# Optimization experiments

Hardware: AMD Instinct MI355X
Metric: run time of the kernel (lower is better)

The kernel has to match this reference:

```python
import jax, jax.numpy as jnp
import numpy as np

B, S, T = 2048, 32, 32
D, H = 128, 256       # cle_dim, rnn_dim
VS, VT = 256, 256     # source/target char vocab
BOW = 1               # MorphoDataset.Factor.BOW


def setup_inputs() -> dict:
    key = jax.random.key(0)
    ks = jax.random.split(key, 16)
    n = lambda k, sh: (jax.random.normal(k, sh, jnp.float32) * 0.05)
    inp = {
        "src_emb": n(ks[0], (VS, D)),
        "tgt_emb": n(ks[1], (VT, D)),
        "enc_f_W": n(ks[2], (D, 3 * H)),
        "enc_f_U": n(ks[3], (H, 3 * H)),
        "enc_f_b": jnp.zeros((2, 3 * H), jnp.float32),
        "enc_b_W": n(ks[4], (D, 3 * H)),
        "enc_b_U": n(ks[5], (H, 3 * H)),
        "enc_b_b": jnp.zeros((2, 3 * H), jnp.float32),
        "dec_W": n(ks[6], (D + H, 3 * H)),
        "dec_U": n(ks[7], (H, 3 * H)),
        "dec_b": jnp.zeros((2, 3 * H), jnp.float32),
        "out_W": n(ks[8], (H, VT)),
        "out_b": jnp.zeros((VT,), jnp.float32),
        "att_src_W": n(ks[9], (H, H)),
        "att_src_b": jnp.zeros((H,), jnp.float32),
        "att_st_W": n(ks[10], (H, H)),
        "att_st_b": jnp.zeros((H,), jnp.float32),
        "att_v": n(ks[11], (H, 1)),
        "att_v_b": jnp.zeros((1,), jnp.float32),
        "source_ids": jax.random.randint(ks[12], (B, S), 0, VS, jnp.int32),
        "target_ids": jax.random.randint(ks[13], (B, T), 0, VT, jnp.int32),
    }
    return inp


def _gru_step(h, x, W, U, b):
    # Keras GRU, reset_after=True: separate input/recurrent biases b[0], b[1]
    gx = x @ W + b[0]
    gh = h @ U + b[1]
    xz, xr, xh = jnp.split(gx, 3, axis=-1)
    hz, hr, hh = jnp.split(gh, 3, axis=-1)
    z = jax.nn.sigmoid(xz + hz)
    r = jax.nn.sigmoid(xr + hr)
    c = jnp.tanh(xh + r * hh)
    return z * h + (1.0 - z) * c


def _gru_scan(x_tbd, W, U, b):
    # x_tbd: [S, B, D] -> outputs [S, B, H]
    h0 = jnp.zeros((x_tbd.shape[1], U.shape[0]), x_tbd.dtype)
    def step(h, x):
        h = _gru_step(h, x, W, U, b)
        return h, h
    _, ys = jax.lax.scan(step, h0, x_tbd)
    return ys


def reference(src_emb, tgt_emb, enc_f_W, enc_f_U, enc_f_b, enc_b_W, enc_b_U, enc_b_b,
              dec_W, dec_U, dec_b, out_W, out_b, att_src_W, att_src_b,
              att_st_W, att_st_b, att_v, att_v_b, source_ids, target_ids):
    # ---- Encoder: bidirectional GRU, merge_mode='sum' ----
    x = src_emb[source_ids]                      # [B, S, D]
    x_t = jnp.transpose(x, (1, 0, 2))            # [S, B, D]
    fwd = _gru_scan(x_t, enc_f_W, enc_f_U, enc_f_b)
    bwd = _gru_scan(x_t[::-1], enc_b_W, enc_b_U, enc_b_b)[::-1]
    source_states = jnp.transpose(fwd + bwd, (1, 0, 2))  # [B, S, H]

    # projected source states are constant across decoder steps -> precompute
    proj_src = source_states @ att_src_W + att_src_b     # [B, S, H]

    def attend(inp, h):
        p = h @ att_st_W + att_st_b                      # [B, H]
        e = jnp.tanh(proj_src + p[:, None, :]) @ att_v + att_v_b  # [B, S, 1]
        w = jax.nn.softmax(e, axis=1)                    # softmax over source positions
        ctx = jnp.sum(source_states * w, axis=1)         # [B, H]
        return jnp.concatenate([inp, ctx], axis=1)       # [B, D+H]

    # ---- Decoder (teacher forcing) ----
    h0 = source_states[:, 0]                             # [B, H]
    bow = jnp.broadcast_to(tgt_emb[BOW], (source_ids.shape[0], tgt_emb.shape[1]))
    inp0 = attend(bow, h0)

    def dstep(carry, tgt_t):
        h, inp = carry
        h = _gru_step(h, inp, dec_W, dec_U, dec_b)       # GRUCell step
        logits = h @ out_W + out_b                       # [B, VT]
        nxt = attend(tgt_emb[tgt_t], h)
        return (h, nxt), logits

    _, logits = jax.lax.scan(dstep, (h0, inp0), jnp.transpose(target_ids))
    return jnp.transpose(logits, (1, 0, 2))              # [B, T, VT]
```

## Files before the change

### kernel.cpp

```cpp
#include <hip/hip_runtime.h>
#include <math.h>

#define B_  2048
#define S_  32
#define T_  32
#define D_  128
#define H_  256
#define G3  768
#define VT_ 256
#define BOW_ 1

typedef __attribute__((ext_vector_type(8))) short short8;
typedef __attribute__((ext_vector_type(4))) float f32x4;
typedef __attribute__((ext_vector_type(8))) unsigned short us8;
typedef unsigned short u16;

__device__ inline u16 f2bf(float x) {
  union { float f; unsigned u; } v; v.f = x;
  unsigned r = v.u + 0x7FFFu + ((v.u >> 16) & 1u);
  return (u16)(r >> 16);
}
__device__ inline float bf2f(u16 b) {
  union { unsigned u; float f; } v; v.u = ((unsigned)b) << 16; return v.f;
}
__device__ inline int swz(int r) { return ((r ^ (r >> 3)) & 7) << 3; }
__device__ inline float sigm(float x) { return 1.f / (1.f + expf(-x)); }

struct TMat { const float* src; u16* dhi; u16* dlo; int R; int C; int tile0; };
struct TPack { TMat m[10]; };

__global__ __launch_bounds__(256)
void wsplit_t(TPack P) {
  int bx = blockIdx.x;
  TMat M = P.m[0];
  #pragma unroll
  for (int i = 1; i < 10; i++) if (bx >= P.m[i].tile0) M = P.m[i];
  int ti = bx - M.tile0;
  int tilesR = M.R >> 6;
  int rt = ti % tilesR, ct = ti / tilesR;
  int r0 = rt * 64, c0 = ct * 64;
  __shared__ float ts[64][65];
  int tid = threadIdx.x;
  int cx = tid & 63, ry = tid >> 6;
  #pragma unroll
  for (int i = 0; i < 16; i++) {
    int r = ry * 16 + i;
    ts[r][cx] = M.src[(size_t)(r0 + r) * M.C + c0 + cx];
  }
  __syncthreads();
  int rx = tid & 63, cy = tid >> 6;
  #pragma unroll
  for (int i = 0; i < 16; i++) {
    int cc = cy * 16 + i;
    float v = ts[rx][cc];
    u16 hi = f2bf(v);
    size_t o = (size_t)(c0 + cc) * M.R + r0 + rx;
    M.dhi[o] = hi;
    M.dlo[o] = f2bf(v - bf2f(hi));
  }
}

__global__ __launch_bounds__(256)
void esplit(const float* a, const float* b, u16* ah, u16* al, u16* bh, u16* bl, int n) {
  int i = blockIdx.x * 256 + threadIdx.x;
  if (i >= 2 * n) return;
  const float* s = (i < n) ? a : b;
  u16* dh = (i < n) ? ah : bh;
  u16* dl = (i < n) ? al : bl;
  int j = (i < n) ? i : i - n;
  float v = s[j];
  u16 hi = f2bf(v);
  dh[j] = hi; dl[j] = f2bf(v - bf2f(hi));
}

struct PLeg {
  const u16* Ahi; const u16* Alo; int lda;
  const u16* Bthi; const u16* Btlo; int ldb;
  const float* bias; void* C; int ldc; int cmode;
  int M, N, K;
};

__global__ __launch_bounds__(256)
void gemm_pl(PLeg l0, PLeg l1) {
  PLeg L = blockIdx.z ? l1 : l0;
  int n0 = blockIdx.x * 128; if (n0 >= L.N) return;
  int m0 = blockIdx.y * 128; if (m0 >= L.M) return;
  __shared__ u16 As[128 * 64];
  __shared__ u16 Bs[128 * 64];
  int tid = threadIdx.x;
  int lane = tid & 63, wv = tid >> 6;
  int wr = (wv >> 1) * 64, wc = (wv & 1) * 64;
  int fr = lane & 15, fk = (lane >> 4) * 8;
  f32x4 acc[4][4];
  #pragma unroll
  for (int m = 0; m < 4; m++)
    #pragma unroll
    for (int n = 0; n < 4; n++) acc[m][n] = (f32x4){0.f, 0.f, 0.f, 0.f};

  int s_row = tid >> 1, s_part = tid & 1;

  for (int k0 = 0; k0 < L.K; k0 += 32) {
    if (k0) __syncthreads();
    int swA = swz(s_row);
    {
      const u16* src = (s_part ? L.Alo : L.Ahi) + (size_t)(m0 + s_row) * L.lda + k0;
      #pragma unroll
      for (int q = 0; q < 4; q++)
        *(us8*)&As[(s_row * 64 + s_part * 32 + q * 8) ^ swA] = *(const us8*)(src + q * 8);
    }
    {
      const u16* src = (s_part ? L.Btlo : L.Bthi) + (size_t)(n0 + s_row) * L.ldb + k0;
      #pragma unroll
      for (int q = 0; q < 4; q++)
        *(us8*)&Bs[(s_row * 64 + s_part * 32 + q * 8) ^ swA] = *(const us8*)(src + q * 8);
    }
    __syncthreads();
    short8 bhi[4], blo[4];
    #pragma unroll
    for (int n = 0; n < 4; n++) {
      int c = wc + n * 16 + fr; int sw = swz(c);
      bhi[n] = *(const short8*)&Bs[(c * 64 + fk) ^ sw];
      blo[n] = *(const short8*)&Bs[(c * 64 + 32 + fk) ^ sw];
    }
    #pragma unroll
    for (int m = 0; m < 4; m++) {
      int r = wr + m * 16 + fr; int sw = swz(r);
      short8 ahi = *(const short8*)&As[(r * 64 + fk) ^ sw];
      short8 alo = *(const short8*)&As[(r * 64 + 32 + fk) ^ sw];
      #pragma unroll
      for (int n = 0; n < 4; n++) {
        acc[m][n] = __builtin_amdgcn_mfma_f32_16x16x32_bf16(ahi, bhi[n], acc[m][n], 0, 0, 0);
        acc[m][n] = __builtin_amdgcn_mfma_f32_16x16x32_bf16(ahi, blo[n], acc[m][n], 0, 0, 0);
        acc[m][n] = __builtin_amdgcn_mfma_f32_16x16x32_bf16(alo, bhi[n], acc[m][n], 0, 0, 0);
      }
    }
  }
  int rbase = (lane >> 4) * 4;
  #pragma unroll
  for (int m = 0; m < 4; m++)
    #pragma unroll
    for (int rr = 0; rr < 4; rr++) {
      int row = m0 + wr + m * 16 + rbase + rr;
      #pragma unroll
      for (int n = 0; n < 4; n++) {
        int col = n0 + wc + n * 16 + fr;
        float v = acc[m][n][rr];
        if (L.bias) v += L.bias[col];
        if (L.cmode == 0)      ((float*)L.C)[(size_t)row * L.ldc + col] = v;
        else if (L.cmode == 1) ((u16*)L.C)[(size_t)row * L.ldc + col] = f2bf(v);
        else {
          size_t o = (((size_t)(row & (B_ - 1))) * T_ + (row >> 11)) * VT_ + col;
          ((float*)L.C)[o] = v;
        }
      }
    }
}

struct GruDesc {
  const u16 *a0H, *a0L;
  const u16 *a1H, *a1L;
  const u16 *a2H, *a2L;
  const u16 *b0H, *b0L;
  const u16 *b1H, *b1L;
  const u16 *b2H, *b2L;
  const float *bias0, *bias1;
  const float *hold;
  const u16 *holdH, *holdL;
  float *hnew;
  u16 *hh, *hl;
  u16 *ssH, *ssL;
  const int *ids;
  int ssmode;
  int sidx, rev;
};

template<int MODE>
__global__ __launch_bounds__(256)
void gru_step(GruDesc d0, GruDesc d1) {
  GruDesc D = blockIdx.z ? d1 : d0;
  constexpr int KT  = MODE ? 640 : 384;
  constexpr int KT8 = KT / 8;
  __shared__ u16 As[2 * 32 * KT];

  int j0 = blockIdx.x * 64;
  int m0 = blockIdx.y * 32;
  int tid = threadIdx.x;
  int lane = tid & 63, wv = tid >> 6;
  int fr = lane & 15, kq = lane >> 4;
  int jn = j0 + wv * 16 + fr;

  constexpr int SLOTS = 2 * 32 * KT8;
  constexpr int PER_T = SLOTS / 256;
  #pragma unroll
  for (int i = 0; i < PER_T; i++) {
    int s = tid + i * 256;
    int p = s / (32 * KT8);
    int rem = s - p * (32 * KT8);
    int row = rem / KT8;
    int kb = rem - row * KT8;
    int k = kb * 8;
    const u16* src;
    if (MODE == 0) {
      if (k < 256) src = (p ? D.a0L : D.a0H) + (size_t)(m0 + row) * 256 + k;
      else {
        int ar = D.ids[(m0 + row) * S_ + (D.rev ? (S_ - 1 - D.sidx) : D.sidx)];
        src = (p ? D.a1L : D.a1H) + (size_t)ar * 128 + (k - 256);
      }
    } else {
      if (k < 256)      src = (p ? D.a0L : D.a0H) + (size_t)(m0 + row) * 256 + k;
      else if (k < 512) src = (p ? D.a1L : D.a1H) + (size_t)(m0 + row) * 256 + (k - 256);
      else {
        int ar = (D.sidx == 0) ? BOW_ : D.ids[(m0 + row) * T_ + D.sidx - 1];
        src = (p ? D.a2L : D.a2H) + (size_t)ar * 128 + (k - 512);
      }
    }
    *(us8*)&As[(s ^ (row & 7)) * 8] = *(const us8*)src;
  }
  __syncthreads();

  f32x4 acc[4][2];
  #pragma unroll
  for (int a = 0; a < 4; a++)
    #pragma unroll
    for (int m = 0; m < 2; m++) acc[a][m] = (f32x4){0.f, 0.f, 0.f, 0.f};

  int arow_slot[2];
  #pragma unroll
  for (int m = 0; m < 2; m++) arow_slot[m] = (m * 16 + fr) * KT8 + kq;

  auto kstep = [&](int k0, int bk, const u16* bHp, const u16* bLp, int ldb, int ai2) {
    short8 ah[2], al[2];
    #pragma unroll
    for (int m = 0; m < 2; m++) {
      int sl = (arow_slot[m] + (k0 >> 3)) ^ (fr & 7);
      ah[m] = *(const short8*)&As[sl * 8];
      sl = (arow_slot[m] + 32 * KT8 + (k0 >> 3)) ^ (fr & 7);
      al[m] = *(const short8*)&As[sl * 8];
    }
    #pragma unroll
    for (int st = 0; st < 3; st++) {
      size_t ro = (size_t)(st * 256 + jn) * ldb + bk + kq * 8;
      short8 bh = *(const short8*)(bHp + ro);
      short8 bl = *(const short8*)(bLp + ro);
      int ai = (st < 2) ? st : ai2;
      #pragma unroll
      for (int m = 0; m < 2; m++) {
        acc[ai][m] = __builtin_amdgcn_mfma_f32_16x16x32_bf16(ah[m], bh, acc[ai][m], 0, 0, 0);
        acc[ai][m] = __builtin_amdgcn_mfma_f32_16x16x32_bf16(ah[m], bl, acc[ai][m], 0, 0, 0);
        acc[ai][m] = __builtin_amdgcn_mfma_f32_16x16x32_bf16(al[m], bh, acc[ai][m], 0, 0, 0);
      }
    }
  };

  #pragma unroll
  for (int k0 = 0; k0 < 256; k0 += 32) kstep(k0, k0, D.b0H, D.b0L, 256, 2);
  if (MODE == 0) {
    #pragma unroll
    for (int k0 = 256; k0 < 384; k0 += 32) kstep(k0, k0 - 256, D.b1H, D.b1L, 128, 3);
  } else {
    #pragma unroll
    for (int k0 = 256; k0 < 512; k0 += 32) kstep(k0, k0 - 256, D.b1H, D.b1L, 256, 3);
    #pragma unroll
    for (int k0 = 512; k0 < 640; k0 += 32) kstep(k0, k0 - 512, D.b2H, D.b2L, 128, 3);
  }

  int rbase = kq * 4;
  int j = jn;
  float bz = D.bias0[j] + D.bias1[j];
  float br = D.bias0[H_ + j] + D.bias1[H_ + j];
  float bxc = D.bias0[2 * H_ + j];
  float bhc = D.bias1[2 * H_ + j];
  #pragma unroll
  for (int m = 0; m < 2; m++)
    #pragma unroll
    for (int rr = 0; rr < 4; rr++) {
      int b = m0 + m * 16 + rbase + rr;
      size_t o = (size_t)b * H_ + j;
      float z = sigm(acc[0][m][rr] + bz);
      float r = sigm(acc[1][m][rr] + br);
      float c = tanhf(acc[3][m][rr] + bxc + r * (acc[2][m][rr] + bhc));
      float hprev = D.hold ? D.hold[o] : (bf2f(D.holdH[o]) + bf2f(D.holdL[o]));
      float hn = z * hprev + (1.f - z) * c;
      D.hnew[o] = hn;
      u16 hi = f2bf(hn);
      D.hh[o] = hi; D.hl[o] = f2bf(hn - bf2f(hi));
      if (MODE == 0) {
        if (D.ssmode == 1) {
          u16 vh = f2bf(hn);
          D.ssH[o] = vh; D.ssL[o] = f2bf(hn - bf2f(vh));
        } else if (D.ssmode == 2) {
          float v = bf2f(D.ssH[o]) + bf2f(D.ssL[o]) + hn;
          u16 vh = f2bf(v);
          D.ssH[o] = vh; D.ssL[o] = f2bf(v - bf2f(vh));
        }
      }
    }
}

__global__ __launch_bounds__(256)
void attend_k(const u16* __restrict__ projbf, const u16* __restrict__ ssH,
              const float* __restrict__ p, const float* __restrict__ att_v,
              u16* __restrict__ ctxh, u16* __restrict__ ctxl) {
  int b = blockIdx.x;
  int tid = threadIdx.x;
  int lane = tid & 63;
  int wv = tid >> 6;
  __shared__ float e_s[S_];
  __shared__ float w_s[S_];
  float pq[4], vq[4];
  #pragma unroll
  for (int q = 0; q < 4; q++) {
    pq[q] = p[(size_t)b * H_ + q * 64 + lane];
    vq[q] = att_v[q * 64 + lane];
  }
  #pragma unroll
  for (int i = 0; i < 8; i++) {
    int s = wv * 8 + i;
    const u16* pr = projbf + ((size_t)s * B_ + b) * H_;
    float part = 0.f;
    #pragma unroll
    for (int q = 0; q < 4; q++)
      part += tanhf(bf2f(pr[q * 64 + lane]) + pq[q]) * vq[q];
    #pragma unroll
    for (int off = 32; off; off >>= 1)
      part += __shfl_xor(part, off);
    if (lane == 0) e_s[s] = part;
  }
  __syncthreads();
  float m = -1e30f;
  #pragma unroll
  for (int s = 0; s < S_; s++) m = fmaxf(m, e_s[s]);
  float den = 0.f;
  #pragma unroll
  for (int s = 0; s < S_; s++) den += expf(e_s[s] - m);
  if (tid < S_) w_s[tid] = expf(e_s[tid] - m) / den;
  __syncthreads();
  float acc = 0.f;
  #pragma unroll
  for (int s = 0; s < S_; s++)
    acc = fmaf(w_s[s], bf2f(ssH[((size_t)s * B_ + b) * H_ + tid]), acc);
  u16 hi = f2bf(acc);
  size_t o = (size_t)b * H_ + tid;
  ctxh[o] = hi; ctxl[o] = f2bf(acc - bf2f(hi));
}

extern "C" void kernel_launch(void* const* d_in, const int* in_sizes, int n_in,
                              void* d_out, int out_size, void* d_ws, size_t ws_size,
                              hipStream_t stream) {
  const float* src_emb   = (const float*)d_in[0];
  const float* tgt_emb   = (const float*)d_in[1];
  const float* enc_f_W   = (const float*)d_in[2];
  const float* enc_f_U   = (const float*)d_in[3];
  const float* enc_f_b   = (const float*)d_in[4];
  const float* enc_b_W   = (const float*)d_in[5];
  const float* enc_b_U   = (const float*)d_in[6];
  const float* enc_b_b   = (const float*)d_in[7];
  const float* dec_W     = (const float*)d_in[8];
  const float* dec_U     = (const float*)d_in[9];
  const float* dec_b     = (const float*)d_in[10];
  const float* out_W     = (const float*)d_in[11];
  const float* out_b     = (const float*)d_in[12];
  const float* att_src_W = (const float*)d_in[13];
  const float* att_src_b = (const float*)d_in[14];
  const float* att_st_W  = (const float*)d_in[15];
  const float* att_st_b  = (const float*)d_in[16];
  const float* att_v     = (const float*)d_in[17];
  const int* source_ids  = (const int*)d_in[19];
  const int* target_ids  = (const int*)d_in[20];
  float* out = (float*)d_out;

  char* base = (char*)d_ws;
  size_t off = 0;
  auto allocB = [&](size_t bytes) { void* p = base + off; off = (off + bytes + 255) & ~255UL; return p; };
  const size_t BH = (size_t)B_ * H_;

  u16* ssH    = (u16*)allocB((size_t)S_ * BH * 2);
  u16* ssL    = (u16*)allocB((size_t)S_ * BH * 2);
  u16* projbf = (u16*)allocB((size_t)S_ * BH * 2);
  float* pbuf = (float*)allocB(BH * 4);
  u16* ctxh = (u16*)allocB(BH * 2);
  u16* ctxl = (u16*)allocB(BH * 2);

  float* encF0 = (float*)allocB(2 * BH * 4);
  u16*  encPl0 = (u16*)allocB(4 * BH * 2);
  float* encF1 = (float*)allocB(2 * BH * 4);
  u16*  encPl1 = (u16*)allocB(4 * BH * 2);
  float* encF[2][2]  = { { encF0, encF0 + BH }, { encF1, encF1 + BH } };
  u16*  encH[2][2]   = { { encPl0, encPl0 + 2 * BH }, { encPl1, encPl1 + 2 * BH } };
  u16*  encL[2][2]   = { { encPl0 + BH, encPl0 + 3 * BH }, { encPl1 + BH, encPl1 + 3 * BH } };

  float* hDecF[2] = { (float*)allocB(BH * 4), (float*)allocB(BH * 4) };
  u16* hAllH = (u16*)allocB((size_t)T_ * BH * 2);
  u16* hAllL = (u16*)allocB((size_t)T_ * BH * 2);

  auto planes2 = [&](size_t n, u16*& h, u16*& l) { h = (u16*)allocB(n * 2); l = (u16*)allocB(n * 2); };
  u16 *UtFh,*UtFl,*UtBh,*UtBl,*WtFh,*WtFl,*WtBh,*WtBl;
  u16 *dUth,*dUtl,*dWcth,*dWctl,*dWxth,*dWxtl;
  u16 *oWth,*oWtl,*aStth,*aSttl,*aSrth,*aSrtl;
  u16 *sEh,*sEl,*tEh,*tEl;
  planes2((size_t)G3*H_, UtFh, UtFl);   planes2((size_t)G3*H_, UtBh, UtBl);
  planes2((size_t)G3*D_, WtFh, WtFl);   planes2((size_t)G3*D_, WtBh, WtBl);
  planes2((size_t)G3*H_, dUth, dUtl);   planes2((size_t)G3*H_, dWcth, dWctl);
  planes2((size_t)G3*D_, dWxth, dWxtl);
  planes2((size_t)H_*VT_, oWth, oWtl);
  planes2((size_t)H_*H_, aStth, aSttl); planes2((size_t)H_*H_, aSrth, aSrtl);
  planes2((size_t)VT_*D_, sEh, sEl);    planes2((size_t)VT_*D_, tEh, tEl);

  TPack P;
  P.m[0] = { enc_f_U,          UtFh, UtFl, 256, 768, 0   };
  P.m[1] = { enc_b_U,          UtBh, UtBl, 256, 768, 48  };
  P.m[2] = { dec_U,            dUth, dUtl, 256, 768, 96  };
  P.m[3] = { dec_W + 128 * G3, dWcth, dWctl, 256, 768, 144 };
  P.m[4] = { enc_f_W,          WtFh, WtFl, 128, 768, 192 };
  P.m[5] = { enc_b_W,          WtBh, WtBl, 128, 768, 216 };
  P.m[6] = { dec_W,            dWxth, dWxtl, 128, 768, 240 };
  P.m[7] = { out_W,            oWth, oWtl, 256, 256, 264 };
  P.m[8] = { att_st_W,         aStth, aSttl, 256, 256, 280 };
  P.m[9] = { att_src_W,        aSrth, aSrtl, 256, 256, 296 };
  wsplit_t<<<312, 256, 0, stream>>>(P);
  esplit<<<(2 * VT_ * D_ + 255) / 256, 256, 0, stream>>>(src_emb, tgt_emb, sEh, sEl, tEh, tEl, VT_ * D_);

  hipMemsetAsync(encF0, 0, 2 * BH * 4, stream);
  hipMemsetAsync(encPl0, 0, 4 * BH * 2, stream);

  for (int s = 0; s < S_; s++) {
    int p = s & 1;
    GruDesc dd[2];
    for (int d = 0; d < 2; d++) {
      GruDesc& D = dd[d];
      D.a0H = encH[p][d]; D.a0L = encL[p][d];
      D.a1H = sEh; D.a1L = sEl;
      D.a2H = nullptr; D.a2L = nullptr;
      D.b0H = d ? UtBh : UtFh; D.b0L = d ? UtBl : UtFl;
      D.b1H = d ? WtBh : WtFh; D.b1L = d ? WtBl : WtFl;
      D.b2H = nullptr; D.b2L = nullptr;
      D.bias0 = d ? enc_b_b : enc_f_b;
      D.bias1 = (d ? enc_b_b : enc_f_b) + G3;
      D.hold = encF[p][d]; D.holdH = nullptr; D.holdL = nullptr;
      D.hnew = encF[p ^ 1][d];
      D.hh = encH[p ^ 1][d]; D.hl = encL[p ^ 1][d];
      int pos = d ? (S_ - 1 - s) : s;
      D.ssH = ssH + (size_t)pos * BH; D.ssL = ssL + (size_t)pos * BH;
      D.ids = source_ids;
      D.ssmode = (s < S_ / 2) ? 1 : 2;
      D.sidx = s; D.rev = d;
    }
    gru_step<0><<<dim3(4, 64, 2), 256, 0, stream>>>(dd[0], dd[1]);
  }

  {
    PLeg proj = { ssH, ssL, H_, aSrth, aSrtl, H_, att_src_b, projbf, H_, 1, S_ * B_, H_, H_ };
    PLeg p0   = { ssH, ssL, H_, aStth, aSttl, H_, att_st_b,  pbuf,   H_, 0, B_,      H_, H_ };
    gemm_pl<<<dim3(2, 512, 2), 256, 0, stream>>>(proj, p0);
  }
  attend_k<<<B_, 256, 0, stream>>>(projbf, ssH, pbuf, att_v, ctxh, ctxl);

  for (int t = 0; t < T_; t++) {
    int p = t & 1;
    GruDesc D = {};
    D.a0H = t ? hAllH + (size_t)(t - 1) * BH : ssH;
    D.a0L = t ? hAllL + (size_t)(t - 1) * BH : ssL;
    D.a1H = ctxh; D.a1L = ctxl;
    D.a2H = tEh;  D.a2L = tEl;
    D.b0H = dUth;  D.b0L = dUtl;
    D.b1H = dWcth; D.b1L = dWctl;
    D.b2H = dWxth; D.b2L = dWxtl;
    D.bias0 = dec_b; D.bias1 = dec_b + G3;
    if (t == 0) { D.hold = nullptr; D.holdH = ssH; D.holdL = ssL; }
    else        { D.hold = hDecF[p]; D.holdH = nullptr; D.holdL = nullptr; }
    D.hnew = hDecF[p ^ 1];
    D.hh = hAllH + (size_t)t * BH; D.hl = hAllL + (size_t)t * BH;
    D.ssH = nullptr; D.ssL = nullptr;
    D.ids = target_ids;
    D.ssmode = 0; D.sidx = t; D.rev = 0;
    gru_step<1><<<dim3(4, 64, 1), 256, 0, stream>>>(D, D);

    if (t < T_ - 1) {
      PLeg LP = { hAllH + (size_t)t * BH, hAllL + (size_t)t * BH, H_,
                  aStth, aSttl, H_, att_st_b, pbuf, H_, 0, B_, H_, H_ };
      gemm_pl<<<dim3(2, 16, 1), 256, 0, stream>>>(LP, LP);
      attend_k<<<B_, 256, 0, stream>>>(projbf, ssH, pbuf, att_v, ctxh, ctxl);
    }
  }

  {
    PLeg LO = { hAllH, hAllL, H_, oWth, oWtl, H_, out_b, out, 0, 2, T_ * B_, VT_, H_ };
    gemm_pl<<<dim3(2, 512, 1), 256, 0, stream>>>(LO, LO);
  }
}
```

Baseline: 3.648 ms.

## Prefetch operands in registers across GEMM, GRU step and attention kernels

The tiled GEMM now loads the next K-chunk from global memory into registers while MFMAs run on the current shared-memory tile, at the cost of an extra barrier per chunk. The GRU step kernel drops its shared-memory staging of A and instead reads A and B fragments straight from global memory with a two-deep register double buffer. The decoder GRU launch now uses 16-row tiles, which doubles the grid. The attention kernel issues all projection and source-state loads up front to expose memory-level parallelism, which raises register pressure.

```diff
diff --git a/kernel.cpp b/kernel.cpp
--- a/kernel.cpp
+++ b/kernel.cpp
@@ -98,29 +98,38 @@
     for (int n = 0; n < 4; n++) acc[m][n] = (f32x4){0.f, 0.f, 0.f, 0.f};
 
   int s_row = tid >> 1, s_part = tid & 1;
-
-  for (int k0 = 0; k0 < L.K; k0 += 32) {
-    if (k0) __syncthreads();
-    int swA = swz(s_row);
-    {
-      const u16* src = (s_part ? L.Alo : L.Ahi) + (size_t)(m0 + s_row) * L.lda + k0;
+  const u16* srcA = (s_part ? L.Alo : L.Ahi) + (size_t)(m0 + s_row) * L.lda;
+  const u16* srcB = (s_part ? L.Btlo : L.Bthi) + (size_t)(n0 + s_row) * L.ldb;
+
+  us8 ra[4], rb[4];
+  #pragma unroll
+  for (int q = 0; q < 4; q++) {
+    ra[q] = *(const us8*)(srcA + q * 8);
+    rb[q] = *(const us8*)(srcB + q * 8);
+  }
+
+  int NC = L.K / 32;
+  int swA = swz(s_row);
+  for (int c = 0; c < NC; c++) {
+    #pragma unroll
+    for (int q = 0; q < 4; q++) {
+      *(us8*)&As[(s_row * 64 + s_part * 32 + q * 8) ^ swA] = ra[q];
+      *(us8*)&Bs[(s_row * 64 + s_part * 32 + q * 8) ^ swA] = rb[q];
+    }
+    __syncthreads();
+    if (c + 1 < NC) {
       #pragma unroll
-      for (int q = 0; q < 4; q++)
-        *(us8*)&As[(s_row * 64 + s_part * 32 + q * 8) ^ swA] = *(const us8*)(src + q * 8);
-    }
-    {
-      const u16* src = (s_part ? L.Btlo : L.Bthi) + (size_t)(n0 + s_row) * L.ldb + k0;
-      #pragma unroll
-      for (int q = 0; q < 4; q++)
-        *(us8*)&Bs[(s_row * 64 + s_part * 32 + q * 8) ^ swA] = *(const us8*)(src + q * 8);
-    }
-    __syncthreads();
+      for (int q = 0; q < 4; q++) {
+        ra[q] = *(const us8*)(srcA + (c + 1) * 32 + q * 8);
+        rb[q] = *(const us8*)(srcB + (c + 1) * 32 + q * 8);
+      }
+    }
     short8 bhi[4], blo[4];
     #pragma unroll
     for (int n = 0; n < 4; n++) {
-      int c = wc + n * 16 + fr; int sw = swz(c);
-      bhi[n] = *(const short8*)&Bs[(c * 64 + fk) ^ sw];
-      blo[n] = *(const short8*)&Bs[(c * 64 + 32 + fk) ^ sw];
+      int cc = wc + n * 16 + fr; int sw = swz(cc);
+      bhi[n] = *(const short8*)&Bs[(cc * 64 + fk) ^ sw];
+      blo[n] = *(const short8*)&Bs[(cc * 64 + 32 + fk) ^ sw];
     }
     #pragma unroll
     for (int m = 0; m < 4; m++) {
@@ -134,6 +143,7 @@
         acc[m][n] = __builtin_amdgcn_mfma_f32_16x16x32_bf16(alo, bhi[n], acc[m][n], 0, 0, 0);
       }
     }
+    __syncthreads();
   }
   int rbase = (lane >> 4) * 4;
   #pragma unroll
@@ -178,107 +188,97 @@
 __global__ __launch_bounds__(256)
 void gru_step(GruDesc d0, GruDesc d1) {
   GruDesc D = blockIdx.z ? d1 : d0;
-  constexpr int KT  = MODE ? 640 : 384;
-  constexpr int KT8 = KT / 8;
-  __shared__ u16 As[2 * 32 * KT];
+  constexpr int MF  = MODE ? 1 : 2;
+  constexpr int NST = MODE ? 20 : 12;
 
   int j0 = blockIdx.x * 64;
-  int m0 = blockIdx.y * 32;
+  int m0 = blockIdx.y * (16 * MF);
   int tid = threadIdx.x;
   int lane = tid & 63, wv = tid >> 6;
   int fr = lane & 15, kq = lane >> 4;
   int jn = j0 + wv * 16 + fr;
 
-  constexpr int SLOTS = 2 * 32 * KT8;
-  constexpr int PER_T = SLOTS / 256;
-  #pragma unroll
-  for (int i = 0; i < PER_T; i++) {
-    int s = tid + i * 256;
-    int p = s / (32 * KT8);
-    int rem = s - p * (32 * KT8);
-    int row = rem / KT8;
-    int kb = rem - row * KT8;
-    int k = kb * 8;
-    const u16* src;
+  int hrow[MF], erow[MF];
+  #pragma unroll
+  for (int mf = 0; mf < MF; mf++) {
+    hrow[mf] = m0 + mf * 16 + fr;
+    if (MODE == 0)
+      erow[mf] = D.ids[hrow[mf] * S_ + (D.rev ? (S_ - 1 - D.sidx) : D.sidx)];
+    else
+      erow[mf] = (D.sidx == 0) ? BOW_ : D.ids[hrow[mf] * T_ + D.sidx - 1];
+  }
+
+  f32x4 acc[4][MF];
+  #pragma unroll
+  for (int a = 0; a < 4; a++)
+    #pragma unroll
+    for (int mf = 0; mf < MF; mf++) acc[a][mf] = (f32x4){0.f, 0.f, 0.f, 0.f};
+
+  short8 pah[2][MF], pal[2][MF], pbh[2][3], pbl[2][3];
+
+  auto loadStep = [&](int i, short8* ah, short8* al, short8* bh3, short8* bl3) {
+    const u16 *BH, *BL, *AH, *AL; int ldb, bk, lda; bool gather;
     if (MODE == 0) {
-      if (k < 256) src = (p ? D.a0L : D.a0H) + (size_t)(m0 + row) * 256 + k;
-      else {
-        int ar = D.ids[(m0 + row) * S_ + (D.rev ? (S_ - 1 - D.sidx) : D.sidx)];
-        src = (p ? D.a1L : D.a1H) + (size_t)ar * 128 + (k - 256);
-      }
+      if (i < 8) { BH = D.b0H; BL = D.b0L; ldb = 256; bk = i * 32;
+                   AH = D.a0H; AL = D.a0L; lda = 256; gather = false; }
+      else       { BH = D.b1H; BL = D.b1L; ldb = 128; bk = (i - 8) * 32;
+                   AH = D.a1H; AL = D.a1L; lda = 128; gather = true; }
     } else {
-      if (k < 256)      src = (p ? D.a0L : D.a0H) + (size_t)(m0 + row) * 256 + k;
-      else if (k < 512) src = (p ? D.a1L : D.a1H) + (size_t)(m0 + row) * 256 + (k - 256);
-      else {
-        int ar = (D.sidx == 0) ? BOW_ : D.ids[(m0 + row) * T_ + D.sidx - 1];
-        src = (p ? D.a2L : D.a2H) + (size_t)ar * 128 + (k - 512);
-      }
-    }
-    *(us8*)&As[(s ^ (row & 7)) * 8] = *(const us8*)src;
-  }
-  __syncthreads();
-
-  f32x4 acc[4][2];
-  #pragma unroll
-  for (int a = 0; a < 4; a++)
-    #pragma unroll
-    for (int m = 0; m < 2; m++) acc[a][m] = (f32x4){0.f, 0.f, 0.f, 0.f};
-
-  int arow_slot[2];
-  #pragma unroll
-  for (int m = 0; m < 2; m++) arow_slot[m] = (m * 16 + fr) * KT8 + kq;
-
-  auto kstep = [&](int k0, int bk, const u16* bHp, const u16* bLp, int ldb, int ai2) {
-    short8 ah[2], al[2];
-    #pragma unroll
-    for (int m = 0; m < 2; m++) {
-      int sl = (arow_slot[m] + (k0 >> 3)) ^ (fr & 7);
-      ah[m] = *(const short8*)&As[sl * 8];
-      sl = (arow_slot[m] + 32 * KT8 + (k0 >> 3)) ^ (fr & 7);
-      al[m] = *(const short8*)&As[sl * 8];
+      if (i < 8)       { BH = D.b0H; BL = D.b0L; ldb = 256; bk = i * 32;
+                         AH = D.a0H; AL = D.a0L; lda = 256; gather = false; }
+      else if (i < 16) { BH = D.b1H; BL = D.b1L; ldb = 256; bk = (i - 8) * 32;
+                         AH = D.a1H; AL = D.a1L; lda = 256; gather = false; }
+      else             { BH = D.b2H; BL = D.b2L; ldb = 128; bk = (i - 16) * 32;
+                         AH = D.a2H; AL = D.a2L; lda = 128; gather = true; }
+    }
+    #pragma unroll
+    for (int mf = 0; mf < MF; mf++) {
+      int r = gather ? erow[mf] : hrow[mf];
+      size_t ao = (size_t)r * lda + bk + kq * 8;
+      ah[mf] = *(const short8*)(AH + ao);
+      al[mf] = *(const short8*)(AL + ao);
     }
     #pragma unroll
     for (int st = 0; st < 3; st++) {
       size_t ro = (size_t)(st * 256 + jn) * ldb + bk + kq * 8;
-      short8 bh = *(const short8*)(bHp + ro);
-      short8 bl = *(const short8*)(bLp + ro);
+      bh3[st] = *(const short8*)(BH + ro);
+      bl3[st] = *(const short8*)(BL + ro);
+    }
+  };
+
+  loadStep(0, pah[0], pal[0], pbh[0], pbl[0]);
+  loadStep(1, pah[1], pal[1], pbh[1], pbl[1]);
+  #pragma unroll
+  for (int i = 0; i < NST; i++) {
+    int ai2 = (i < 8) ? 2 : 3;
+    #pragma unroll
+    for (int st = 0; st < 3; st++) {
       int ai = (st < 2) ? st : ai2;
       #pragma unroll
-      for (int m = 0; m < 2; m++) {
-        acc[ai][m] = __builtin_amdgcn_mfma_f32_16x16x32_bf16(ah[m], bh, acc[ai][m], 0, 0, 0);
-        acc[ai][m] = __builtin_amdgcn_mfma_f32_16x16x32_bf16(ah[m], bl, acc[ai][m], 0, 0, 0);
-        acc[ai][m] = __builtin_amdgcn_mfma_f32_16x16x32_bf16(al[m], bh, acc[ai][m], 0, 0, 0);
+      for (int mf = 0; mf < MF; mf++) {
+        acc[ai][mf] = __builtin_amdgcn_mfma_f32_16x16x32_bf16(pah[i & 1][mf], pbh[i & 1][st], acc[ai][mf], 0, 0, 0);
+        acc[ai][mf] = __builtin_amdgcn_mfma_f32_16x16x32_bf16(pah[i & 1][mf], pbl[i & 1][st], acc[ai][mf], 0, 0, 0);
+        acc[ai][mf] = __builtin_amdgcn_mfma_f32_16x16x32_bf16(pal[i & 1][mf], pbh[i & 1][st], acc[ai][mf], 0, 0, 0);
       }
     }
-  };
-
-  #pragma unroll
-  for (int k0 = 0; k0 < 256; k0 += 32) kstep(k0, k0, D.b0H, D.b0L, 256, 2);
-  if (MODE == 0) {
-    #pragma unroll
-    for (int k0 = 256; k0 < 384; k0 += 32) kstep(k0, k0 - 256, D.b1H, D.b1L, 128, 3);
-  } else {
-    #pragma unroll
-    for (int k0 = 256; k0 < 512; k0 += 32) kstep(k0, k0 - 256, D.b1H, D.b1L, 256, 3);
-    #pragma unroll
-    for (int k0 = 512; k0 < 640; k0 += 32) kstep(k0, k0 - 512, D.b2H, D.b2L, 128, 3);
+    if (i + 2 < NST) loadStep(i + 2, pah[i & 1], pal[i & 1], pbh[i & 1], pbl[i & 1]);
   }
 
   int rbase = kq * 4;
   int j = jn;
-  float bz = D.bias0[j] + D.bias1[j];
-  float br = D.bias0[H_ + j] + D.bias1[H_ + j];
+  float bz  = D.bias0[j] + D.bias1[j];
+  float br  = D.bias0[H_ + j] + D.bias1[H_ + j];
   float bxc = D.bias0[2 * H_ + j];
   float bhc = D.bias1[2 * H_ + j];
   #pragma unroll
-  for (int m = 0; m < 2; m++)
+  for (int mf = 0; mf < MF; mf++)
     #pragma unroll
     for (int rr = 0; rr < 4; rr++) {
-      int b = m0 + m * 16 + rbase + rr;
+      int b = m0 + mf * 16 + rbase + rr;
       size_t o = (size_t)b * H_ + j;
-      float z = sigm(acc[0][m][rr] + bz);
-      float r = sigm(acc[1][m][rr] + br);
-      float c = tanhf(acc[3][m][rr] + bxc + r * (acc[2][m][rr] + bhc));
+      float z = sigm(acc[0][mf][rr] + bz);
+      float r = sigm(acc[1][mf][rr] + br);
+      float c = tanhf(acc[3][mf][rr] + bxc + r * (acc[2][mf][rr] + bhc));
       float hprev = D.hold ? D.hold[o] : (bf2f(D.holdH[o]) + bf2f(D.holdL[o]));
       float hn = z * hprev + (1.f - z) * c;
       D.hnew[o] = hn;
@@ -313,18 +313,27 @@
     pq[q] = p[(size_t)b * H_ + q * 64 + lane];
     vq[q] = att_v[q * 64 + lane];
   }
+  float pv[8][4];
   #pragma unroll
   for (int i = 0; i < 8; i++) {
-    int s = wv * 8 + i;
-    const u16* pr = projbf + ((size_t)s * B_ + b) * H_;
+    const u16* pr = projbf + ((size_t)(wv * 8 + i) * B_ + b) * H_;
+    #pragma unroll
+    for (int q = 0; q < 4; q++) pv[i][q] = bf2f(pr[q * 64 + lane]);
+  }
+  u16 sv[S_];
+  #pragma unroll
+  for (int s = 0; s < S_; s++) sv[s] = ssH[((size_t)s * B_ + b) * H_ + tid];
+
+  #pragma unroll
+  for (int i = 0; i < 8; i++) {
     float part = 0.f;
     #pragma unroll
     for (int q = 0; q < 4; q++)
-      part += tanhf(bf2f(pr[q * 64 + lane]) + pq[q]) * vq[q];
+      part += tanhf(pv[i][q] + pq[q]) * vq[q];
     #pragma unroll
     for (int off = 32; off; off >>= 1)
       part += __shfl_xor(part, off);
-    if (lane == 0) e_s[s] = part;
+    if (lane == 0) e_s[wv * 8 + i] = part;
   }
   __syncthreads();
   float m = -1e30f;
@@ -338,7 +347,7 @@
   float acc = 0.f;
   #pragma unroll
   for (int s = 0; s < S_; s++)
-    acc = fmaf(w_s[s], bf2f(ssH[((size_t)s * B_ + b) * H_ + tid]), acc);
+    acc = fmaf(w_s[s], bf2f(sv[s]), acc);
   u16 hi = f2bf(acc);
   size_t o = (size_t)b * H_ + tid;
   ctxh[o] = hi; ctxl[o] = f2bf(acc - bf2f(hi));
@@ -473,7 +482,7 @@
     D.ssH = nullptr; D.ssL = nullptr;
     D.ids = target_ids;
     D.ssmode = 0; D.sidx = t; D.rev = 0;
-    gru_step<1><<<dim3(4, 64, 1), 256, 0, stream>>>(D, D);
+    gru_step<1><<<dim3(4, 128, 1), 256, 0, stream>>>(D, D);
 
     if (t < T_ - 1) {
       PLeg LP = { hAllH + (size_t)t * BH, hAllL + (size_t)t * BH, H_,
```

Measured after the change: 4.116 ms. 1.13x slower.

## Precompute embedding-gate tables, fuse attention projection into attend, retile decoder GRU

Applied to the files above, without the earlier changes.

Since inputs are one-hot vocab lookups, the x@W gate contributions are precomputed once per vocab entry into fp32 tables (VT x 768) and gathered in the GRU epilogue, shrinking K from 384 to 256 (encoder) and 640 to 512 (decoder). The per-step att_st projection GEMM and the attend kernel are fused into one lp_attend kernel that handles 8 batch rows per block, using a plain fp32 FMA loop. The decoder GRU grid doubles its column tiles with a single M fragment per wave to raise block count. This cuts launches and redundant GEMM work per step. In exchange it adds scattered table gathers in the epilogue and a scalar fp32 projection loop in the attention kernel.

```diff
diff --git a/kernel.cpp b/kernel.cpp
--- a/kernel.cpp
+++ b/kernel.cpp
@@ -9,6 +9,7 @@
 #define G3  768
 #define VT_ 256
 #define BOW_ 1
+#define NB  8
 
 typedef __attribute__((ext_vector_type(8))) short short8;
 typedef __attribute__((ext_vector_type(4))) float f32x4;
@@ -118,9 +119,9 @@
     short8 bhi[4], blo[4];
     #pragma unroll
     for (int n = 0; n < 4; n++) {
-      int c = wc + n * 16 + fr; int sw = swz(c);
-      bhi[n] = *(const short8*)&Bs[(c * 64 + fk) ^ sw];
-      blo[n] = *(const short8*)&Bs[(c * 64 + 32 + fk) ^ sw];
+      int cc = wc + n * 16 + fr; int sw = swz(cc);
+      bhi[n] = *(const short8*)&Bs[(cc * 64 + fk) ^ sw];
+      blo[n] = *(const short8*)&Bs[(cc * 64 + 32 + fk) ^ sw];
     }
     #pragma unroll
     for (int m = 0; m < 4; m++) {
@@ -159,10 +160,9 @@
 struct GruDesc {
   const u16 *a0H, *a0L;
   const u16 *a1H, *a1L;
-  const u16 *a2H, *a2L;
   const u16 *b0H, *b0L;
   const u16 *b1H, *b1L;
-  const u16 *b2H, *b2L;
+  const float *gxT;
   const float *bias0, *bias1;
   const float *hold;
   const u16 *holdH, *holdL;
@@ -178,19 +178,21 @@
 __global__ __launch_bounds__(256)
 void gru_step(GruDesc d0, GruDesc d1) {
   GruDesc D = blockIdx.z ? d1 : d0;
-  constexpr int KT  = MODE ? 640 : 384;
+  constexpr int KT  = MODE ? 512 : 256;
   constexpr int KT8 = KT / 8;
-  __shared__ u16 As[2 * 32 * KT];
-
-  int j0 = blockIdx.x * 64;
+  constexpr int MF  = MODE ? 1 : 2;
+  constexpr int NST = KT / 32;
+  __shared__ __align__(16) u16 As[2 * 32 * KT];
+
   int m0 = blockIdx.y * 32;
   int tid = threadIdx.x;
   int lane = tid & 63, wv = tid >> 6;
   int fr = lane & 15, kq = lane >> 4;
-  int jn = j0 + wv * 16 + fr;
-
-  constexpr int SLOTS = 2 * 32 * KT8;
-  constexpr int PER_T = SLOTS / 256;
+  int jn, rb0;
+  if (MODE == 0) { jn = blockIdx.x * 64 + wv * 16 + fr; rb0 = 0; }
+  else           { jn = blockIdx.x * 32 + (wv & 1) * 16 + fr; rb0 = (wv >> 1) * 16; }
+
+  constexpr int PER_T = (2 * 32 * KT8) / 256;
   #pragma unroll
   for (int i = 0; i < PER_T; i++) {
     int s = tid + i * 256;
@@ -201,84 +203,69 @@
     int k = kb * 8;
     const u16* src;
     if (MODE == 0) {
-      if (k < 256) src = (p ? D.a0L : D.a0H) + (size_t)(m0 + row) * 256 + k;
-      else {
-        int ar = D.ids[(m0 + row) * S_ + (D.rev ? (S_ - 1 - D.sidx) : D.sidx)];
-        src = (p ? D.a1L : D.a1H) + (size_t)ar * 128 + (k - 256);
+      src = (p ? D.a0L : D.a0H) + (size_t)(m0 + row) * 256 + k;
+    } else {
+      src = (k < 256) ? (p ? D.a0L : D.a0H) + (size_t)(m0 + row) * 256 + k
+                      : (p ? D.a1L : D.a1H) + (size_t)(m0 + row) * 256 + (k - 256);
+    }
+    *(us8*)&As[(s ^ (row & 7)) * 8] = *(const us8*)src;
+  }
+  __syncthreads();
+
+  f32x4 acc[4][MF];
+  #pragma unroll
+  for (int a = 0; a < 4; a++)
+    #pragma unroll
+    for (int mf = 0; mf < MF; mf++) acc[a][mf] = (f32x4){0.f, 0.f, 0.f, 0.f};
+
+  #pragma unroll
+  for (int i = 0; i < NST; i++) {
+    const u16 *BH, *BL; int bk, ai2;
+    if (MODE == 0)    { BH = D.b0H; BL = D.b0L; bk = i * 32; ai2 = 2; }
+    else if (i < 8)   { BH = D.b0H; BL = D.b0L; bk = i * 32; ai2 = 2; }
+    else              { BH = D.b1H; BL = D.b1L; bk = (i - 8) * 32; ai2 = 3; }
+    short8 ah[MF], al[MF];
+    #pragma unroll
+    for (int mf = 0; mf < MF; mf++) {
+      int rp = rb0 + mf * 16 + fr;
+      int kb = i * 4 + kq;
+      ah[mf] = *(const short8*)&As[((rp * KT8 + kb) ^ (fr & 7)) * 8];
+      al[mf] = *(const short8*)&As[((32 * KT8 + rp * KT8 + kb) ^ (fr & 7)) * 8];
+    }
+    #pragma unroll
+    for (int st = 0; st < 3; st++) {
+      size_t ro = (size_t)(st * 256 + jn) * 256 + bk + kq * 8;
+      short8 bh = *(const short8*)(BH + ro);
+      short8 bl = *(const short8*)(BL + ro);
+      int ai = (st < 2) ? st : ai2;
+      #pragma unroll
+      for (int mf = 0; mf < MF; mf++) {
+        acc[ai][mf] = __builtin_amdgcn_mfma_f32_16x16x32_bf16(ah[mf], bh, acc[ai][mf], 0, 0, 0);
+        acc[ai][mf] = __builtin_amdgcn_mfma_f32_16x16x32_bf16(ah[mf], bl, acc[ai][mf], 0, 0, 0);
+        acc[ai][mf] = __builtin_amdgcn_mfma_f32_16x16x32_bf16(al[mf], bh, acc[ai][mf], 0, 0, 0);
       }
-    } else {
-      if (k < 256)      src = (p ? D.a0L : D.a0H) + (size_t)(m0 + row) * 256 + k;
-      else if (k < 512) src = (p ? D.a1L : D.a1H) + (size_t)(m0 + row) * 256 + (k - 256);
-      else {
-        int ar = (D.sidx == 0) ? BOW_ : D.ids[(m0 + row) * T_ + D.sidx - 1];
-        src = (p ? D.a2L : D.a2H) + (size_t)ar * 128 + (k - 512);
-      }
-    }
-    *(us8*)&As[(s ^ (row & 7)) * 8] = *(const us8*)src;
-  }
-  __syncthreads();
-
-  f32x4 acc[4][2];
-  #pragma unroll
-  for (int a = 0; a < 4; a++)
-    #pragma unroll
-    for (int m = 0; m < 2; m++) acc[a][m] = (f32x4){0.f, 0.f, 0.f, 0.f};
-
-  int arow_slot[2];
-  #pragma unroll
-  for (int m = 0; m < 2; m++) arow_slot[m] = (m * 16 + fr) * KT8 + kq;
-
-  auto kstep = [&](int k0, int bk, const u16* bHp, const u16* bLp, int ldb, int ai2) {
-    short8 ah[2], al[2];
-    #pragma unroll
-    for (int m = 0; m < 2; m++) {
-      int sl = (arow_slot[m] + (k0 >> 3)) ^ (fr & 7);
-      ah[m] = *(const short8*)&As[sl * 8];
-      sl = (arow_slot[m] + 32 * KT8 + (k0 >> 3)) ^ (fr & 7);
-      al[m] = *(const short8*)&As[sl * 8];
-    }
-    #pragma unroll
-    for (int st = 0; st < 3; st++) {
-      size_t ro = (size_t)(st * 256 + jn) * ldb + bk + kq * 8;
-      short8 bh = *(const short8*)(bHp + ro);
-      short8 bl = *(const short8*)(bLp + ro);
-      int ai = (st < 2) ? st : ai2;
-      #pragma unroll
-      for (int m = 0; m < 2; m++) {
-        acc[ai][m] = __builtin_amdgcn_mfma_f32_16x16x32_bf16(ah[m], bh, acc[ai][m], 0, 0, 0);
-        acc[ai][m] = __builtin_amdgcn_mfma_f32_16x16x32_bf16(ah[m], bl, acc[ai][m], 0, 0, 0);
-        acc[ai][m] = __builtin_amdgcn_mfma_f32_16x16x32_bf16(al[m], bh, acc[ai][m], 0, 0, 0);
-      }
-    }
-  };
-
-  #pragma unroll
-  for (int k0 = 0; k0 < 256; k0 += 32) kstep(k0, k0, D.b0H, D.b0L, 256, 2);
-  if (MODE == 0) {
-    #pragma unroll
-    for (int k0 = 256; k0 < 384; k0 += 32) kstep(k0, k0 - 256, D.b1H, D.b1L, 128, 3);
-  } else {
-    #pragma unroll
-    for (int k0 = 256; k0 < 512; k0 += 32) kstep(k0, k0 - 256, D.b1H, D.b1L, 256, 3);
-    #pragma unroll
-    for (int k0 = 512; k0 < 640; k0 += 32) kstep(k0, k0 - 512, D.b2H, D.b2L, 128, 3);
+    }
   }
 
   int rbase = kq * 4;
   int j = jn;
-  float bz = D.bias0[j] + D.bias1[j];
-  float br = D.bias0[H_ + j] + D.bias1[H_ + j];
-  float bxc = D.bias0[2 * H_ + j];
-  float bhc = D.bias1[2 * H_ + j];
-  #pragma unroll
-  for (int m = 0; m < 2; m++)
+  float b0z = D.bias0[j],       b1z = D.bias1[j];
+  float b0r = D.bias0[256 + j], b1r = D.bias1[256 + j];
+  float b0c = D.bias0[512 + j], b1c = D.bias1[512 + j];
+  #pragma unroll
+  for (int mf = 0; mf < MF; mf++)
     #pragma unroll
     for (int rr = 0; rr < 4; rr++) {
-      int b = m0 + m * 16 + rbase + rr;
+      int b = m0 + rb0 + mf * 16 + rbase + rr;
       size_t o = (size_t)b * H_ + j;
-      float z = sigm(acc[0][m][rr] + bz);
-      float r = sigm(acc[1][m][rr] + br);
-      float c = tanhf(acc[3][m][rr] + bxc + r * (acc[2][m][rr] + bhc));
+      int id;
+      if (MODE == 0) id = D.ids[b * S_ + (D.rev ? (S_ - 1 - D.sidx) : D.sidx)];
+      else           id = (D.sidx == 0) ? BOW_ : D.ids[b * T_ + D.sidx - 1];
+      const float* T = D.gxT + (size_t)id * G3;
+      float z = sigm(acc[0][mf][rr] + T[j] + b0z + b1z);
+      float r = sigm(acc[1][mf][rr] + T[256 + j] + b0r + b1r);
+      float xc = T[512 + j] + b0c + (MODE ? acc[3][mf][rr] : 0.f);
+      float c = tanhf(xc + r * (acc[2][mf][rr] + b1c));
       float hprev = D.hold ? D.hold[o] : (bf2f(D.holdH[o]) + bf2f(D.holdL[o]));
       float hn = z * hprev + (1.f - z) * c;
       D.hnew[o] = hn;
@@ -286,8 +273,7 @@
       D.hh[o] = hi; D.hl[o] = f2bf(hn - bf2f(hi));
       if (MODE == 0) {
         if (D.ssmode == 1) {
-          u16 vh = f2bf(hn);
-          D.ssH[o] = vh; D.ssL[o] = f2bf(hn - bf2f(vh));
+          D.ssH[o] = hi; D.ssL[o] = f2bf(hn - bf2f(hi));
         } else if (D.ssmode == 2) {
           float v = bf2f(D.ssH[o]) + bf2f(D.ssL[o]) + hn;
           u16 vh = f2bf(v);
@@ -298,50 +284,78 @@
 }
 
 __global__ __launch_bounds__(256)
-void attend_k(const u16* __restrict__ projbf, const u16* __restrict__ ssH,
-              const float* __restrict__ p, const float* __restrict__ att_v,
-              u16* __restrict__ ctxh, u16* __restrict__ ctxl) {
-  int b = blockIdx.x;
+void lp_attend(const u16* __restrict__ hH, const u16* __restrict__ hL,
+               const float* __restrict__ stW, const float* __restrict__ stb,
+               const u16* __restrict__ projbf, const u16* __restrict__ ssH,
+               const float* __restrict__ att_v,
+               u16* __restrict__ ctxh, u16* __restrict__ ctxl) {
+  int b0 = blockIdx.x * NB;
   int tid = threadIdx.x;
-  int lane = tid & 63;
-  int wv = tid >> 6;
-  __shared__ float e_s[S_];
-  __shared__ float w_s[S_];
-  float pq[4], vq[4];
-  #pragma unroll
-  for (int q = 0; q < 4; q++) {
-    pq[q] = p[(size_t)b * H_ + q * 64 + lane];
-    vq[q] = att_v[q * 64 + lane];
-  }
-  #pragma unroll
-  for (int i = 0; i < 8; i++) {
-    int s = wv * 8 + i;
-    const u16* pr = projbf + ((size_t)s * B_ + b) * H_;
-    float part = 0.f;
-    #pragma unroll
-    for (int q = 0; q < 4; q++)
-      part += tanhf(bf2f(pr[q * 64 + lane]) + pq[q]) * vq[q];
-    #pragma unroll
-    for (int off = 32; off; off >>= 1)
-      part += __shfl_xor(part, off);
-    if (lane == 0) e_s[s] = part;
+  int lane = tid & 63, wv = tid >> 6;
+  __shared__ float hsh[NB][H_];
+  __shared__ float ps[NB][H_];
+  __shared__ float ews[NB][S_];
+  #pragma unroll
+  for (int bb = 0; bb < NB; bb++) {
+    size_t o = (size_t)(b0 + bb) * H_ + tid;
+    hsh[bb][tid] = bf2f(hH[o]) + bf2f(hL[o]);
   }
   __syncthreads();
-  float m = -1e30f;
-  #pragma unroll
-  for (int s = 0; s < S_; s++) m = fmaxf(m, e_s[s]);
-  float den = 0.f;
-  #pragma unroll
-  for (int s = 0; s < S_; s++) den += expf(e_s[s] - m);
-  if (tid < S_) w_s[tid] = expf(e_s[tid] - m) / den;
+  float p[NB];
+  float pb = stb[tid];
+  #pragma unroll
+  for (int bb = 0; bb < NB; bb++) p[bb] = pb;
+  for (int k = 0; k < H_; k++) {
+    float w = stW[(size_t)k * H_ + tid];
+    #pragma unroll
+    for (int bb = 0; bb < NB; bb++) p[bb] = fmaf(hsh[bb][k], w, p[bb]);
+  }
+  #pragma unroll
+  for (int bb = 0; bb < NB; bb++) ps[bb][tid] = p[bb];
   __syncthreads();
-  float acc = 0.f;
-  #pragma unroll
-  for (int s = 0; s < S_; s++)
-    acc = fmaf(w_s[s], bf2f(ssH[((size_t)s * B_ + b) * H_ + tid]), acc);
-  u16 hi = f2bf(acc);
-  size_t o = (size_t)b * H_ + tid;
-  ctxh[o] = hi; ctxl[o] = f2bf(acc - bf2f(hi));
+  float vq[4];
+  #pragma unroll
+  for (int q = 0; q < 4; q++) vq[q] = att_v[q * 64 + lane];
+  #pragma unroll
+  for (int u = 0; u < 2; u++) {
+    int bb = wv * 2 + u;
+    float pq[4];
+    #pragma unroll
+    for (int q = 0; q < 4; q++) pq[q] = ps[bb][q * 64 + lane];
+    for (int s = 0; s < S_; s++) {
+      const u16* pr = projbf + ((size_t)s * B_ + b0 + bb) * H_;
+      float part = 0.f;
+      #pragma unroll
+      for (int q = 0; q < 4; q++)
+        part += tanhf(bf2f(pr[q * 64 + lane]) + pq[q]) * vq[q];
+      #pragma unroll
+      for (int off = 32; off; off >>= 1) part += __shfl_xor(part, off);
+      if (lane == 0) ews[bb][s] = part;
+    }
+  }
+  __syncthreads();
+  if (tid < NB) {
+    float m = -1e30f;
+    #pragma unroll
+    for (int s = 0; s < S_; s++) m = fmaxf(m, ews[tid][s]);
+    float ex[S_]; float den = 0.f;
+    #pragma unroll
+    for (int s = 0; s < S_; s++) { ex[s] = expf(ews[tid][s] - m); den += ex[s]; }
+    float inv = 1.f / den;
+    #pragma unroll
+    for (int s = 0; s < S_; s++) ews[tid][s] = ex[s] * inv;
+  }
+  __syncthreads();
+  #pragma unroll
+  for (int bb = 0; bb < NB; bb++) {
+    float acc = 0.f;
+    #pragma unroll
+    for (int s = 0; s < S_; s++)
+      acc = fmaf(ews[bb][s], bf2f(ssH[((size_t)s * B_ + b0 + bb) * H_ + tid]), acc);
+    u16 hi = f2bf(acc);
+    size_t o = (size_t)(b0 + bb) * H_ + tid;
+    ctxh[o] = hi; ctxl[o] = f2bf(acc - bf2f(hi));
+  }
 }
 
 extern "C" void kernel_launch(void* const* d_in, const int* in_sizes, int n_in,
@@ -377,7 +391,6 @@
   u16* ssH    = (u16*)allocB((size_t)S_ * BH * 2);
   u16* ssL    = (u16*)allocB((size_t)S_ * BH * 2);
   u16* projbf = (u16*)allocB((size_t)S_ * BH * 2);
-  float* pbuf = (float*)allocB(BH * 4);
   u16* ctxh = (u16*)allocB(BH * 2);
   u16* ctxl = (u16*)allocB(BH * 2);
 
@@ -396,15 +409,18 @@
   auto planes2 = [&](size_t n, u16*& h, u16*& l) { h = (u16*)allocB(n * 2); l = (u16*)allocB(n * 2); };
   u16 *UtFh,*UtFl,*UtBh,*UtBl,*WtFh,*WtFl,*WtBh,*WtBl;
   u16 *dUth,*dUtl,*dWcth,*dWctl,*dWxth,*dWxtl;
-  u16 *oWth,*oWtl,*aStth,*aSttl,*aSrth,*aSrtl;
+  u16 *oWth,*oWtl,*aSrth,*aSrtl;
   u16 *sEh,*sEl,*tEh,*tEl;
   planes2((size_t)G3*H_, UtFh, UtFl);   planes2((size_t)G3*H_, UtBh, UtBl);
   planes2((size_t)G3*D_, WtFh, WtFl);   planes2((size_t)G3*D_, WtBh, WtBl);
   planes2((size_t)G3*H_, dUth, dUtl);   planes2((size_t)G3*H_, dWcth, dWctl);
   planes2((size_t)G3*D_, dWxth, dWxtl);
   planes2((size_t)H_*VT_, oWth, oWtl);
-  planes2((size_t)H_*H_, aStth, aSttl); planes2((size_t)H_*H_, aSrth, aSrtl);
+  planes2((size_t)H_*H_, aSrth, aSrtl);
   planes2((size_t)VT_*D_, sEh, sEl);    planes2((size_t)VT_*D_, tEh, tEl);
+  float* Tf = (float*)allocB((size_t)VT_ * G3 * 4);
+  float* Tb = (float*)allocB((size_t)VT_ * G3 * 4);
+  float* Td = (float*)allocB((size_t)VT_ * G3 * 4);
 
   TPack P;
   P.m[0] = { enc_f_U,          UtFh, UtFl, 256, 768, 0   };
@@ -415,10 +431,18 @@
   P.m[5] = { enc_b_W,          WtBh, WtBl, 128, 768, 216 };
   P.m[6] = { dec_W,            dWxth, dWxtl, 128, 768, 240 };
   P.m[7] = { out_W,            oWth, oWtl, 256, 256, 264 };
-  P.m[8] = { att_st_W,         aStth, aSttl, 256, 256, 280 };
-  P.m[9] = { att_src_W,        aSrth, aSrtl, 256, 256, 296 };
-  wsplit_t<<<312, 256, 0, stream>>>(P);
+  P.m[8] = { att_src_W,        aSrth, aSrtl, 256, 256, 280 };
+  P.m[9] = { att_src_W,        aSrth, aSrtl, 256, 256, 1 << 30 };
+  wsplit_t<<<296, 256, 0, stream>>>(P);
   esplit<<<(2 * VT_ * D_ + 255) / 256, 256, 0, stream>>>(src_emb, tgt_emb, sEh, sEl, tEh, tEl, VT_ * D_);
+
+  {
+    PLeg tf = { sEh, sEl, D_, WtFh, WtFl, D_, nullptr, Tf, G3, 0, VT_, G3, D_ };
+    PLeg tb = { sEh, sEl, D_, WtBh, WtBl, D_, nullptr, Tb, G3, 0, VT_, G3, D_ };
+    gemm_pl<<<dim3(6, 2, 2), 256, 0, stream>>>(tf, tb);
+    PLeg td = { tEh, tEl, D_, dWxth, dWxtl, D_, nullptr, Td, G3, 0, VT_, G3, D_ };
+    gemm_pl<<<dim3(6, 2, 1), 256, 0, stream>>>(td, td);
+  }
 
   hipMemsetAsync(encF0, 0, 2 * BH * 4, stream);
   hipMemsetAsync(encPl0, 0, 4 * BH * 2, stream);
@@ -429,11 +453,10 @@
     for (int d = 0; d < 2; d++) {
       GruDesc& D = dd[d];
       D.a0H = encH[p][d]; D.a0L = encL[p][d];
-      D.a1H = sEh; D.a1L = sEl;
-      D.a2H = nullptr; D.a2L = nullptr;
+      D.a1H = nullptr; D.a1L = nullptr;
       D.b0H = d ? UtBh : UtFh; D.b0L = d ? UtBl : UtFl;
-      D.b1H = d ? WtBh : WtFh; D.b1L = d ? WtBl : WtFl;
-      D.b2H = nullptr; D.b2L = nullptr;
+      D.b1H = nullptr; D.b1L = nullptr;
+      D.gxT = d ? Tb : Tf;
       D.bias0 = d ? enc_b_b : enc_f_b;
       D.bias1 = (d ? enc_b_b : enc_f_b) + G3;
       D.hold = encF[p][d]; D.holdH = nullptr; D.holdL = nullptr;
@@ -450,10 +473,10 @@
 
   {
     PLeg proj = { ssH, ssL, H_, aSrth, aSrtl, H_, att_src_b, projbf, H_, 1, S_ * B_, H_, H_ };
-    PLeg p0   = { ssH, ssL, H_, aStth, aSttl, H_, att_st_b,  pbuf,   H_, 0, B_,      H_, H_ };
-    gemm_pl<<<dim3(2, 512, 2), 256, 0, stream>>>(proj, p0);
-  }
-  attend_k<<<B_, 256, 0, stream>>>(projbf, ssH, pbuf, att_v, ctxh, ctxl);
+    gemm_pl<<<dim3(2, 512, 1), 256, 0, stream>>>(proj, proj);
+  }
+  lp_attend<<<B_ / NB, 256, 0, stream>>>(ssH, ssL, att_st_W, att_st_b,
+                                         projbf, ssH, att_v, ctxh, ctxl);
 
   for (int t = 0; t < T_; t++) {
     int p = t & 1;
@@ -461,10 +484,9 @@
     D.a0H = t ? hAllH + (size_t)(t - 1) * BH : ssH;
     D.a0L = t ? hAllL + (size_t)(t - 1) * BH : ssL;
     D.a1H = ctxh; D.a1L = ctxl;
-    D.a2H = tEh;  D.a2L = tEl;
     D.b0H = dUth;  D.b0L = dUtl;
     D.b1H = dWcth; D.b1L = dWctl;
-    D.b2H = dWxth; D.b2L = dWxtl;
+    D.gxT = Td;
     D.bias0 = dec_b; D.bias1 = dec_b + G3;
     if (t == 0) { D.hold = nullptr; D.holdH = ssH; D.holdL = ssL; }
     else        { D.hold = hDecF[p]; D.holdH = nullptr; D.holdL = nullptr; }
@@ -473,14 +495,12 @@
     D.ssH = nullptr; D.ssL = nullptr;
     D.ids = target_ids;
     D.ssmode = 0; D.sidx = t; D.rev = 0;
-    gru_step<1><<<dim3(4, 64, 1), 256, 0, stream>>>(D, D);
-
-    if (t < T_ - 1) {
-      PLeg LP = { hAllH + (size_t)t * BH, hAllL + (size_t)t * BH, H_,
-                  aStth, aSttl, H_, att_st_b, pbuf, H_, 0, B_, H_, H_ };
-      gemm_pl<<<dim3(2, 16, 1), 256, 0, stream>>>(LP, LP);
-      attend_k<<<B_, 256, 0, stream>>>(projbf, ssH, pbuf, att_v, ctxh, ctxl);
-    }
+    gru_step<1><<<dim3(8, 64, 1), 256, 0, stream>>>(D, D);
+
+    if (t < T_ - 1)
+      lp_attend<<<B_ / NB, 256, 0, stream>>>(hAllH + (size_t)t * BH, hAllL + (size_t)t * BH,
+                                             att_st_W, att_st_b,
+                                             projbf, ssH, att_v, ctxh, ctxl);
   }
 
   {
```

New measurement: 7.153 ms. +96.1%, slower.
